# Kernel tuning notes

Hardware: AMD Instinct MI355X
Metric: run time of the kernel (lower is better)

The kernel has to match this reference:

```python
import jax, jax.numpy as jnp
import numpy as np

B, C, H, W = 256, 512, 14, 14
HW = H * W
TAU = 0.03          # args.tau
EPS = 0.65          # args.epsilon
EPS2 = 0.40         # args.epsilon - args.epsilon_margin
T_LOGIT = 0.07      # args.logit_temperature
MAX_ITERS = 32      # static unrolled bound for the data-dependent while-loop
PD_EPS = 1e-6       # torch.nn.PairwiseDistance default eps (added to the difference)


def setup_inputs() -> dict:
    key = jax.random.key(0)
    k1, k2 = jax.random.split(key)
    img = jax.random.normal(k1, (B, C, H, W), jnp.float32)
    img = img / (jnp.linalg.norm(img, axis=1, keepdims=True) + 1e-12)  # L2 over channels
    aud = jax.random.normal(k2, (B, C), jnp.float32)
    aud = aud / (jnp.linalg.norm(aud, axis=1, keepdims=True) + 1e-12)
    return {"img": img, "aud": aud}


def reference(img, aud):
    Bb, Cc, Hh, Ww = img.shape
    n_pix = Hh * Ww

    # PosLogits: [B,1,H,W]; Alllogits: [B,B,H,W]
    pos_logits = jnp.einsum('ncqa,nc->nqa', img, aud)[:, None]
    all_logits = jnp.einsum('ncqa,kc->nkqa', img, aud)

    # trimap negatives
    pos2 = jax.nn.sigmoid((pos_logits - EPS2) / TAU)
    neg = 1.0 - pos2                                        # [B,1,H,W]

    logit = img.reshape(Bb, Cc, -1) * pos_logits.reshape(Bb, 1, -1)   # [B,C,HW]
    positive0 = pos_logits.reshape(Bb, -1)                            # [B,HW]
    neg_val = (logit * neg.reshape(Bb, 1, -1)).mean(axis=2)           # [B,C]

    logit_t = logit.transpose(0, 2, 1)                                 # [B,HW,C]
    dist_to_zero = jnp.linalg.norm(logit_t - neg_val[:, None, :] + PD_EPS, axis=-1)  # [B,HW]

    def body(t, state):
        positive, already_pos, endpoint, obj = state
        idx = jnp.argmax(positive, axis=1)                             # [B] (detached in torch)
        sel = jnp.take_along_axis(logit, idx[:, None, None], axis=2)[:, :, 0]  # [B,C]
        obj = obj.at[t].set(sel * (~endpoint)[:, None].astype(sel.dtype))
        dist_to_logit = jnp.linalg.norm(logit_t - sel[:, None, :] + PD_EPS, axis=-1)  # [B,HW]
        pos = (dist_to_logit < dist_to_zero) & (~already_pos)
        already_pos = already_pos | pos
        positive = positive * (1.0 - pos.astype(positive.dtype))
        endpoint = endpoint | (pos.sum(axis=1) == 0) | (positive.max(axis=1) < 0.1)
        return (positive, already_pos, endpoint, obj)

    obj0 = jnp.zeros((MAX_ITERS, Bb, Cc), img.dtype)
    state0 = (positive0,
              jnp.zeros((Bb, n_pix), bool),
              jnp.zeros((Bb,), bool),
              obj0)
    _, _, _, object_arr = jax.lax.fori_loop(0, MAX_ITERS, body, state0)

    # lvs contrastive loss
    mask = 1.0 - 100.0 * jnp.eye(Bb, dtype=img.dtype)
    pos_m = jax.nn.sigmoid((pos_logits - EPS) / TAU)                   # [B,1,H,W]
    pos_all = jax.nn.sigmoid((all_logits - EPS) / TAU)                 # [B,B,H,W]
    sim1 = (pos_m * pos_logits).reshape(Bb, 1, -1).sum(-1) / pos_m.reshape(Bb, 1, -1).sum(-1)
    sim = (pos_all * all_logits).reshape(Bb, Bb, -1).sum(-1) / pos_all.reshape(Bb, Bb, -1).sum(-1) * mask
    sim2 = (neg * pos_logits).reshape(Bb, 1, -1).sum(-1) / neg.reshape(Bb, 1, -1).sum(-1)
    logits = jnp.concatenate((sim1, sim, sim2), axis=1) / T_LOGIT      # [B, B+2]
    loss = -jax.nn.log_softmax(logits, axis=1)[:, 0].mean()           # CE with target 0

    return loss, pos_logits[:, 0], object_arr
```

## Files before the change

kernel.cpp:

```cpp
#include <hip/hip_runtime.h>
#include <hip/hip_bf16.h>
#include <math.h>

#define NB 256
#define NC 512
#define NP 196
#define NIT 32
#define PROWS 208
#define PR 196
#define LSTR 72
#define SFSTR 211

typedef __attribute__((ext_vector_type(8))) short bf16x8;
typedef __attribute__((ext_vector_type(4))) float f32x4;

__device__ __forceinline__ float sigf(float z){ return 1.0f/(1.0f+expf(-z)); }

__device__ __forceinline__ unsigned short f2bf(float x){
  return __bfloat16_as_ushort(__float2bfloat16(x));
}
__device__ __forceinline__ float bf2f(unsigned short h){
  union{float f; unsigned u;} v; v.u = ((unsigned)h)<<16; return v.f;
}
__device__ __forceinline__ double dshfl_xor(double v, int m){
  int lo = __shfl_xor(__double2loint(v), m);
  int hi = __shfl_xor(__double2hiint(v), m);
  return __hiloint2double(hi, lo);
}


__global__ __launch_bounds__(512) void convert4_kernel(
    const float* __restrict__ img, const float* __restrict__ aud,
    unsigned short* __restrict__ hiT, unsigned short* __restrict__ loT,
    unsigned short* __restrict__ aud_bf,
    double* __restrict__ ppl, double* __restrict__ pcs)
{
  const int bid = blockIdx.x;
  const int b = bid & 255, part = bid >> 8;
  const int tid = threadIdx.x;
  const float* imgb = img + (size_t)b*NC*NP + (size_t)part*64*NP;
  __shared__ float sf[64*SFSTR];
  __shared__ float s_aud[64];
  if (part == 0) aud_bf[b*NC + tid] = f2bf(aud[b*NC + tid]);
  if (tid < 64) s_aud[tid] = aud[b*NC + part*64 + tid];

  for (int j=tid; j<64*49; j+=512){
    int p4 = j % 49, c = j / 49;
    float4 v = *(const float4*)&imgb[(size_t)c*NP + p4*4];
    sf[c*SFSTR + p4*4+0]=v.x; sf[c*SFSTR + p4*4+1]=v.y;
    sf[c*SFSTR + p4*4+2]=v.z; sf[c*SFSTR + p4*4+3]=v.w;
  }
  __syncthreads();

  unsigned short* hp = hiT + (size_t)(b*8+part)*PR*64;
  unsigned short* lp = loT + (size_t)(b*8+part)*PR*64;
  for (int j=tid; j<PROWS*8; j+=512){
    int p = j>>3, o = j&7;
    unsigned hw[4], lw[4];
    double dot=0.0, sm=0.0;
    #pragma unroll
    for (int k2=0;k2<4;++k2){
      int c = o*8 + 2*k2;
      float x0 = (p<NP) ? sf[c*SFSTR + p]     : 0.f;
      float x1 = (p<NP) ? sf[(c+1)*SFSTR + p] : 0.f;
      unsigned short h0=f2bf(x0), h1=f2bf(x1);
      unsigned short l0=f2bf(x0-bf2f(h0)), l1=f2bf(x1-bf2f(h1));
      hw[k2] = (unsigned)h0 | ((unsigned)h1<<16);
      lw[k2] = (unsigned)l0 | ((unsigned)l1<<16);
      dot += (double)x0*(double)s_aud[c] + (double)x1*(double)s_aud[c+1];
      sm  += (double)x0 + (double)x1;
    }
    if (p < NP){
      *(uint4*)&hp[p*64 + o*8] = *(uint4*)hw;
      *(uint4*)&lp[p*64 + o*8] = *(uint4*)lw;
    }
    dot += dshfl_xor(dot,1); dot += dshfl_xor(dot,2); dot += dshfl_xor(dot,4);
    sm  += dshfl_xor(sm,1);  sm  += dshfl_xor(sm,2);  sm  += dshfl_xor(sm,4);
    if (o==0 && p<NP){
      ppl[(size_t)(b*8+part)*NP + p] = dot;
      pcs[(size_t)(b*8+part)*NP + p] = sm;
    }
  }
}

__global__ __launch_bounds__(512) void gram2_kernel(
    const unsigned short* __restrict__ hiT, const unsigned short* __restrict__ loT,
    float* __restrict__ G)
{
  const int bid = blockIdx.x;
  const int slot = bid & 7, seq = bid >> 3;
  const int b = slot + 8*(seq>>1), h = seq & 1;
  const int cbase = 7*h, ncl = 7 - h;
  const int tid = threadIdx.x, lane = tid & 63, w = tid >> 6;
  const int nr = (w<5)?2:1;
  const unsigned short* hb = hiT + (size_t)b*8*PR*64;
  const unsigned short* lb = loT + (size_t)b*8*PR*64;
  float* Gb = G + (size_t)b*NP*NP;
  __shared__ short smh[PROWS*LSTR];
  __shared__ short sml[PROWS*LSTR];

  f32x4 acc[2][7];
  #pragma unroll
  for (int i=0;i<2;++i)
    #pragma unroll
    for (int j=0;j<7;++j) acc[i][j]=(f32x4){0,0,0,0};

  for (int sl=0; sl<8; ++sl){
    __syncthreads();
    for (int j=tid; j<PROWS*8; j+=512){
      int p = j>>3, o = j&7;
      size_t src = ((size_t)sl*PR + p)*64 + o*8;
      *(uint4*)&smh[p*LSTR + o*8] = *(const uint4*)(hb + src);
      *(uint4*)&sml[p*LSTR + o*8] = *(const uint4*)(lb + src);
    }
    __syncthreads();
    #pragma unroll
    for (int kk=0; kk<2; ++kk){
      bf16x8 Ah[2], Al[2];
      #pragma unroll
      for (int i=0;i<2;++i){
        if (i<nr){
          int r = (w + 8*i)*16 + (lane&15);
          Ah[i] = *(const bf16x8*)&smh[r*LSTR + kk*32 + (lane>>4)*8];
          Al[i] = *(const bf16x8*)&sml[r*LSTR + kk*32 + (lane>>4)*8];
        }
      }
      #pragma unroll
      for (int j=0;j<7;++j){
        if (j<ncl){
          int r = (cbase+j)*16 + (lane&15);
          bf16x8 Bh = *(const bf16x8*)&smh[r*LSTR + kk*32 + (lane>>4)*8];
          bf16x8 Bl = *(const bf16x8*)&sml[r*LSTR + kk*32 + (lane>>4)*8];
          #pragma unroll
          for (int i=0;i<2;++i){
            if (i<nr){
              acc[i][j] = __builtin_amdgcn_mfma_f32_16x16x32_bf16(Ah[i], Bh, acc[i][j], 0,0,0);
              acc[i][j] = __builtin_amdgcn_mfma_f32_16x16x32_bf16(Ah[i], Bl, acc[i][j], 0,0,0);
              acc[i][j] = __builtin_amdgcn_mfma_f32_16x16x32_bf16(Al[i], Bh, acc[i][j], 0,0,0);
            }
          }
        }
      }
    }
  }

  const int r0 = (lane>>4)*4, colL = lane & 15;
  #pragma unroll
  for (int i=0;i<2;++i){
    #pragma unroll
    for (int j=0;j<7;++j){
      if (i<nr && j<ncl){
        int row = (w+8*i)*16 + r0;
        int col = (cbase+j)*16 + colL;
        if (col < NP){
          #pragma unroll
          for (int jj=0;jj<4;++jj){
            if (row+jj < NP) Gb[(size_t)(row+jj)*NP + col] = acc[i][j][jj];
          }
        }
      }
    }
  }
}

__global__ __launch_bounds__(1024) void loop6_kernel(
    const double* __restrict__ ppl, const double* __restrict__ pcs,
    const float* __restrict__ G,
    const unsigned short* __restrict__ hiT, const unsigned short* __restrict__ loT,
    float* __restrict__ pl, float* __restrict__ out_pl,
    float* __restrict__ obj)
{
  const int b = blockIdx.x, tid = threadIdx.x, lane = tid & 63, w = tid >> 6;
  const float* Gb = G + (size_t)b*NP*NP;
  __shared__ float sG[NP*NP];
  __shared__ float s_pl[NP], s_wl[NP], s_csL[NP], s_gd[NP];
  __shared__ double gwd[NP];
  __shared__ double s_wred[16];
  __shared__ double s_bc;
  __shared__ int s_q[NIT]; __shared__ int s_z[NIT];

  #pragma unroll
  for (int k=0;k<10;++k){
    int j = k*1024 + tid;
    if (j < NP*NP/4) ((float4*)sG)[j] = ((const float4*)Gb)[j];
  }
  float negw_t = 0.f;
  if (tid < NP){
    double a=0.0, s=0.0;
    #pragma unroll
    for (int part=0; part<8; ++part){
      a += ppl[(size_t)(b*8+part)*NP + tid];
      s += pcs[(size_t)(b*8+part)*NP + tid];
    }
    float plv=(float)a;
    float csv=(float)s;
    pl[b*NP+tid]=plv; out_pl[b*NP+tid]=plv;
    s_pl[tid] = plv;
    s_csL[tid] = plv*csv;
    negw_t = 1.0f - sigf((plv-0.40f)/0.03f);
    s_wl[tid] = plv*negw_t;
    s_gd[tid] = Gb[(size_t)tid*NP + tid];
  }
  __syncthreads();

  {
    int p = tid >> 2, qg = tid & 3;
    double a = 0.0;
    if (p < NP){
      for (int q=qg*49; q<qg*49+49; ++q) a += (double)sG[q*NP + p] * (double)s_wl[q];
    }
    a += dshfl_xor(a,1); a += dshfl_xor(a,2);
    if (qg==0 && p<NP) gwd[p] = a;
  }
  __syncthreads();

  double r = (tid<NP) ? (double)s_wl[tid]*gwd[tid] : 0.0;
  #pragma unroll
  for (int m=1;m<64;m<<=1) r += dshfl_xor(r,m);
  if (lane==0) s_wred[w] = r;
  __syncthreads();
  if (tid==0){ double t=0.0; for (int i=0;i<16;++i) t += s_wred[i]; s_bc = t; }
  __syncthreads();
  const double S2 = s_bc;
  __syncthreads();

  r = (tid<NP) ? (double)negw_t*(double)s_csL[tid] : 0.0;
  #pragma unroll
  for (int m=1;m<64;m<<=1) r += dshfl_xor(r,m);
  if (lane==0) s_wred[w] = r;
  __syncthreads();
  if (tid==0){ double t=0.0; for (int i=0;i<16;++i) t += s_wred[i]; s_bc = t; }
  __syncthreads();
  const double Swl = s_bc;
  __syncthreads();

  if (tid < NP){
    const double e = (double)1e-6f;
    double pld = (double)s_pl[tid];
    double d0sq = pld*pld*(double)s_gd[tid]
                - (2.0/196.0)*pld*gwd[tid]
                + S2/(196.0*196.0)
                + 2.0*e*((double)s_csL[tid] - Swl/196.0)
                + 512.0*e*e;
    if (d0sq < 0.0) d0sq = 0.0;
    gwd[tid] = d0sq;
  }
  __syncthreads();

  if (w == 0){
    float plv[4], csL[4], gdd[4], posv[4];
    double d0sq[4];
    bool alr[4];
    #pragma unroll
    for (int s=0;s<4;++s){
      int p = lane + 64*s;
      bool valid = p < NP;
      plv[s]  = valid ? s_pl[p]  : 0.f;
      csL[s]  = valid ? s_csL[p] : 0.f;
      gdd[s]  = valid ? s_gd[p]  : 0.f;
      d0sq[s] = valid ? gwd[p]   : 0.0;
      posv[s] = valid ? plv[s]   : -INFINITY;
      alr[s] = false;
    }
    bool endp = false;

    for (int t=0;t<NIT;++t){
      float v = posv[0]; int ix = lane;
      #pragma unroll
      for (int s=1;s<4;++s){
        if (posv[s] > v){ v = posv[s]; ix = lane + 64*s; }
      }
      #pragma unroll
      for (int m=1;m<64;m<<=1){
        float vv = __shfl_xor(v, m);
        int   ii = __shfl_xor(ix, m);
        if (vv>v || (vv==v && ii<ix)){ v=vv; ix=ii; }
      }
      const int q = ix;
      const float plq  = s_pl[q];
      const float gqq  = s_gd[q];
      const float csLq = s_csL[q];
      if (lane==0){ s_q[t] = q; s_z[t] = endp ? 1 : 0; }

      int cnt = 0;
      #pragma unroll
      for (int s=0;s<4;++s){
        int p = lane + 64*s;
        if (p<NP && !alr[s]){
          float Gpq = sG[q*NP + p];
          double plp=(double)plv[s], dq=(double)plq;
          const double e=(double)1e-6f;
          double d2 = plp*plp*(double)gdd[s]
                    - 2.0*plp*dq*(double)Gpq
                    + dq*dq*(double)gqq
                    + 2.0*e*((double)csL[s]-(double)csLq)
                    + 512.0*e*e;
          if (d2<0.0) d2=0.0;
          if (d2 < d0sq[s]){ alr[s]=true; posv[s]=posv[s]*0.0f; cnt++; }
        }
      }
      float mx = fmaxf(fmaxf(posv[0],posv[1]),fmaxf(posv[2],posv[3]));
      #pragma unroll
      for (int m=1;m<64;m<<=1){
        cnt += __shfl_xor(cnt, m);
        mx = fmaxf(mx, __shfl_xor(mx, m));
      }
      if (cnt==0 || mx<0.1f) endp=true;
    }
  }
  __syncthreads();

  for (int j=tid; j<NIT*64; j+=1024){
    int t = j >> 6, l8 = j & 63;
    int part = l8 >> 3, off = l8 & 7;
    float o8[8];
    if (s_z[t]){
      #pragma unroll
      for (int e=0;e<8;++e) o8[e]=0.f;
    } else {
      int q = s_q[t];
      float plq = s_pl[q];
      size_t src = ((size_t)(b*8+part)*PR + q)*64 + off*8;
      uint4 hv = *(const uint4*)(hiT + src);
      uint4 lv = *(const uint4*)(loT + src);
      const unsigned* hw = (const unsigned*)&hv;
      const unsigned* lw = (const unsigned*)&lv;
      #pragma unroll
      for (int k2=0;k2<4;++k2){
        float x0 = bf2f((unsigned short)(hw[k2]&0xffff)) + bf2f((unsigned short)(lw[k2]&0xffff));
        float x1 = bf2f((unsigned short)(hw[k2]>>16))    + bf2f((unsigned short)(lw[k2]>>16));
        o8[2*k2]   = x0*plq;
        o8[2*k2+1] = x1*plq;
      }
    }
    float* op = obj + ((size_t)t*NB + b)*NC + l8*8;
    *(float4*)&op[0] = *(float4*)&o8[0];
    *(float4*)&op[4] = *(float4*)&o8[4];
  }
}

__global__ __launch_bounds__(512) void simgemm2_kernel(
    const unsigned short* __restrict__ hiT, const unsigned short* __restrict__ aud_bf,
    float* __restrict__ sumWA, float* __restrict__ sumW)
{
  const int bid = blockIdx.x;
  const int slot = bid & 7, seq = bid >> 3;
  const int b = slot + 8*(seq>>1), h = seq & 1;
  const int tid = threadIdx.x, lane = tid & 63, w = tid >> 6;
  const int wr = w >> 2, wc = w & 3;
  const int pbase = (wr==0)?0:7, npt = 7-wr;
  const unsigned short* hb = hiT + (size_t)b*8*PR*64;
  __shared__ short smh[PROWS*LSTR];
  __shared__ short sma[128*LSTR];
  __shared__ float sred[2][2][4][2][16];

  f32x4 acc[7][2];
  #pragma unroll
  for (int i=0;i<7;++i)
    #pragma unroll
    for (int n=0;n<2;++n) acc[i][n]=(f32x4){0,0,0,0};

  for (int sl=0; sl<8; ++sl){
    __syncthreads();
    for (int j=tid; j<PROWS*8; j+=512){
      int p = j>>3, o = j&7;
      *(uint4*)&smh[p*LSTR + o*8] = *(const uint4*)(hb + ((size_t)sl*PR + p)*64 + o*8);
    }
    for (int j=tid; j<128*8; j+=512){
      int n = j>>3, o = j&7;
      *(uint4*)&sma[n*LSTR + o*8] = *(const uint4*)(aud_bf + (size_t)(h*128+n)*NC + sl*64 + o*8);
    }
    __syncthreads();
    #pragma unroll
    for (int kk=0; kk<2; ++kk){
      bf16x8 Ah[7];
      #pragma unroll
      for (int i=0;i<7;++i){
        if (i<npt){
          int r = (pbase+i)*16 + (lane&15);
          Ah[i] = *(const bf16x8*)&smh[r*LSTR + kk*32 + (lane>>4)*8];
        }
      }
      #pragma unroll
      for (int n=0;n<2;++n){
        int r = (wc*2+n)*16 + (lane&15);
        bf16x8 Bn = *(const bf16x8*)&sma[r*LSTR + kk*32 + (lane>>4)*8];
        #pragma unroll
        for (int i=0;i<7;++i)
          if (i<npt)
            acc[i][n] = __builtin_amdgcn_mfma_f32_16x16x32_bf16(Ah[i], Bn, acc[i][n], 0,0,0);
      }
    }
  }

  float swa[2]={0,0}, sw[2]={0,0};
  #pragma unroll
  for (int n=0;n<2;++n){
    #pragma unroll
    for (int i=0;i<7;++i){
      if (i<npt){
        int rowbase = (pbase+i)*16 + (lane>>4)*4;
        #pragma unroll
        for (int jj=0;jj<4;++jj){
          if (rowbase+jj < NP){
            float v = acc[i][n][jj];
            float wgt = sigf((v-0.65f)/0.03f);
            swa[n] += wgt*v; sw[n] += wgt;
          }
        }
      }
    }
  }
  #pragma unroll
  for (int n=0;n<2;++n){
    swa[n] += __shfl_xor(swa[n],16); swa[n] += __shfl_xor(swa[n],32);
    sw[n]  += __shfl_xor(sw[n],16);  sw[n]  += __shfl_xor(sw[n],32);
  }
  if (lane < 16){
    #pragma unroll
    for (int n=0;n<2;++n){
      sred[0][wr][wc][n][lane] = swa[n];
      sred[1][wr][wc][n][lane] = sw[n];
    }
  }
  __syncthreads();
  if (tid < 128){
    int wc2 = tid>>5, n2 = (tid>>4)&1, col = tid&15;
    float a = sred[0][0][wc2][n2][col] + sred[0][1][wc2][n2][col];
    float s = sred[1][0][wc2][n2][col] + sred[1][1][wc2][n2][col];
    int kcol = h*128 + (wc2*2+n2)*16 + col;
    sumWA[(size_t)b*NB + kcol] = a;
    sumW [(size_t)b*NB + kcol] = s;
  }
}

__global__ __launch_bounds__(256) void finalize_b2(
    const float* __restrict__ pl,
    const float* __restrict__ sumWA, const float* __restrict__ sumW,
    float* __restrict__ lossb)
{
  const int b = blockIdx.x, k = threadIdx.x;
  __shared__ float s_red[256];
  __shared__ double s_redd[256];

  float plv = (k<NP)? pl[b*NP+k] : 0.f;
  float pmw = (k<NP)? sigf((plv-0.65f)/0.03f) : 0.f;
  float negw= (k<NP)? 1.0f - sigf((plv-0.40f)/0.03f) : 0.f;
  double rr[4];
  rr[0]=(k<NP)?(double)pmw*(double)plv:0.0;
  rr[1]=(k<NP)?(double)pmw:0.0;
  rr[2]=(k<NP)?(double)negw*(double)plv:0.0;
  rr[3]=(k<NP)?(double)negw:0.0;
  double res[4];
  for (int i=0;i<4;++i){
    __syncthreads();
    s_redd[k]=rr[i];
    __syncthreads();
    for (int s=128;s>0;s>>=1){ if (k<s) s_redd[k]+=s_redd[k+s]; __syncthreads(); }
    res[i]=s_redd[0];
  }
  const float sim1v = (float)(res[0]/res[1]);
  const float sim2v = (float)(res[2]/res[3]);
  __syncthreads();

  const float T = 0.07f;
  float s = sumWA[(size_t)b*NB+k]/sumW[(size_t)b*NB+k];
  if (k==b) s *= -99.0f;
  const float lk = s/T;
  const float l0 = sim1v/T, ll = sim2v/T;
  s_red[k]=lk; __syncthreads();
  for (int st=128;st>0;st>>=1){ if(k<st) s_red[k]=fmaxf(s_red[k],s_red[k+st]); __syncthreads(); }
  const float m = fmaxf(s_red[0], fmaxf(l0,ll));
  __syncthreads();
  double e = (double)expf(lk-m);
  if (k==0) e += (double)expf(l0-m)+(double)expf(ll-m);
  s_redd[k]=e; __syncthreads();
  for (int st=128;st>0;st>>=1){ if(k<st) s_redd[k]+=s_redd[k+st]; __syncthreads(); }
  if (k==0) lossb[b] = -(float)((double)(l0-m) - log(s_redd[0]));
}

__global__ __launch_bounds__(256) void finalize_sum(const float* __restrict__ lossb, float* __restrict__ out_loss)
{
  const int tid = threadIdx.x;
  __shared__ double sr[256];
  sr[tid]=(double)lossb[tid]; __syncthreads();
  for (int st=128;st>0;st>>=1){ if(tid<st) sr[tid]+=sr[tid+st]; __syncthreads(); }
  if (tid==0) out_loss[0]=(float)(sr[0]/256.0);
}

extern "C" void kernel_launch(void* const* d_in, const int* in_sizes, int n_in,
                              void* d_out, int out_size, void* d_ws, size_t ws_size,
                              hipStream_t stream)
{
  const float* img = (const float*)d_in[0];
  const float* aud = (const float*)d_in[1];
  float* out = (float*)d_out;
  float* ws  = (float*)d_ws;

  float* pl    = ws;
  unsigned short* aud_bf = (unsigned short*)(pl + NB*NP);
  unsigned short* hiT = aud_bf + NB*NC;
  unsigned short* loT = hiT + (size_t)NB*8*PR*64;
  float* G     = (float*)(loT + (size_t)NB*8*PR*64);
  double* ppl  = (double*)(G + (size_t)NB*NP*NP);
  double* pcs  = ppl + (size_t)NB*8*NP;
  float* lossb = (float*)(pcs + (size_t)NB*8*NP);

  float* sumWA = (float*)ppl;
  float* sumW  = sumWA + NB*NB;

  float* out_loss = out;
  float* out_pl   = out + 1;
  float* out_obj  = out + 1 + NB*NP;

  hipLaunchKernelGGL(convert4_kernel, dim3(NB*8),  dim3(512),  0, stream, img, aud, hiT, loT, aud_bf, ppl, pcs);
  hipLaunchKernelGGL(gram2_kernel,    dim3(NB*2),  dim3(512),  0, stream, hiT, loT, G);
  hipLaunchKernelGGL(loop6_kernel,    dim3(NB),    dim3(1024), 0, stream, ppl, pcs, G, hiT, loT, pl, out_pl, out_obj);
  hipLaunchKernelGGL(simgemm2_kernel, dim3(NB*2),  dim3(512),  0, stream, hiT, aud_bf, sumWA, sumW);
  hipLaunchKernelGGL(finalize_b2,     dim3(NB),    dim3(256),  0, stream, pl, sumWA, sumW, lossb);
  hipLaunchKernelGGL(finalize_sum,    dim3(1),     dim3(256),  0, stream, lossb, out_loss);
}
```

Before: 189.6 us.

## Fuse gram and similarity GEMMs into one kernel sharing staged hiT tiles

Merges the Gram-matrix GEMM and the audio-similarity GEMM into a single kernel that loads each hiT slice into LDS once and feeds both MFMA accumulations. This removes a separate kernel launch and a second full read of hiT from global memory. The sumWA/sumW buffers move to a dedicated workspace region since ppl is still live when they are written. The fused kernel holds more accumulators and LDS per block, which may reduce occupancy.

```diff
diff --git a/kernel.cpp b/kernel.cpp
--- a/kernel.cpp
+++ b/kernel.cpp
@@ -83,27 +83,37 @@
   }
 }
 
-__global__ __launch_bounds__(512) void gram2_kernel(
+__global__ __launch_bounds__(512) void gramsim3_kernel(
     const unsigned short* __restrict__ hiT, const unsigned short* __restrict__ loT,
-    float* __restrict__ G)
+    const unsigned short* __restrict__ aud_bf,
+    float* __restrict__ G, float* __restrict__ sumWA, float* __restrict__ sumW)
 {
   const int bid = blockIdx.x;
   const int slot = bid & 7, seq = bid >> 3;
   const int b = slot + 8*(seq>>1), h = seq & 1;
+  const int tid = threadIdx.x, lane = tid & 63, w = tid >> 6;
   const int cbase = 7*h, ncl = 7 - h;
-  const int tid = threadIdx.x, lane = tid & 63, w = tid >> 6;
   const int nr = (w<5)?2:1;
+  const int wr = w >> 2, wc = w & 3;
+  const int pbase = (wr==0)?0:7, npt = 7-wr;
   const unsigned short* hb = hiT + (size_t)b*8*PR*64;
   const unsigned short* lb = loT + (size_t)b*8*PR*64;
   float* Gb = G + (size_t)b*NP*NP;
   __shared__ short smh[PROWS*LSTR];
   __shared__ short sml[PROWS*LSTR];
-
-  f32x4 acc[2][7];
+  __shared__ short sma[128*LSTR];
+  __shared__ float sred[2][2][4][2][16];
+
+  f32x4 gacc[2][7];
   #pragma unroll
   for (int i=0;i<2;++i)
     #pragma unroll
-    for (int j=0;j<7;++j) acc[i][j]=(f32x4){0,0,0,0};
+    for (int j=0;j<7;++j) gacc[i][j]=(f32x4){0,0,0,0};
+  f32x4 sacc[7][2];
+  #pragma unroll
+  for (int i=0;i<7;++i)
+    #pragma unroll
+    for (int n=0;n<2;++n) sacc[i][n]=(f32x4){0,0,0,0};
 
   for (int sl=0; sl<8; ++sl){
     __syncthreads();
@@ -113,53 +123,120 @@
       *(uint4*)&smh[p*LSTR + o*8] = *(const uint4*)(hb + src);
       *(uint4*)&sml[p*LSTR + o*8] = *(const uint4*)(lb + src);
     }
+    for (int j=tid; j<128*8; j+=512){
+      int n = j>>3, o = j&7;
+      *(uint4*)&sma[n*LSTR + o*8] = *(const uint4*)(aud_bf + (size_t)(h*128+n)*NC + sl*64 + o*8);
+    }
     __syncthreads();
     #pragma unroll
     for (int kk=0; kk<2; ++kk){
-      bf16x8 Ah[2], Al[2];
-      #pragma unroll
-      for (int i=0;i<2;++i){
-        if (i<nr){
-          int r = (w + 8*i)*16 + (lane&15);
-          Ah[i] = *(const bf16x8*)&smh[r*LSTR + kk*32 + (lane>>4)*8];
-          Al[i] = *(const bf16x8*)&sml[r*LSTR + kk*32 + (lane>>4)*8];
-        }
-      }
-      #pragma unroll
-      for (int j=0;j<7;++j){
-        if (j<ncl){
-          int r = (cbase+j)*16 + (lane&15);
-          bf16x8 Bh = *(const bf16x8*)&smh[r*LSTR + kk*32 + (lane>>4)*8];
-          bf16x8 Bl = *(const bf16x8*)&sml[r*LSTR + kk*32 + (lane>>4)*8];
-          #pragma unroll
-          for (int i=0;i<2;++i){
-            if (i<nr){
-              acc[i][j] = __builtin_amdgcn_mfma_f32_16x16x32_bf16(Ah[i], Bh, acc[i][j], 0,0,0);
-              acc[i][j] = __builtin_amdgcn_mfma_f32_16x16x32_bf16(Ah[i], Bl, acc[i][j], 0,0,0);
-              acc[i][j] = __builtin_amdgcn_mfma_f32_16x16x32_bf16(Al[i], Bh, acc[i][j], 0,0,0);
+      {
+        bf16x8 Ah[2], Al[2];
+        #pragma unroll
+        for (int i=0;i<2;++i){
+          if (i<nr){
+            int r = (w + 8*i)*16 + (lane&15);
+            Ah[i] = *(const bf16x8*)&smh[r*LSTR + kk*32 + (lane>>4)*8];
+            Al[i] = *(const bf16x8*)&sml[r*LSTR + kk*32 + (lane>>4)*8];
+          }
+        }
+        #pragma unroll
+        for (int j=0;j<7;++j){
+          if (j<ncl){
+            int r = (cbase+j)*16 + (lane&15);
+            bf16x8 Bh = *(const bf16x8*)&smh[r*LSTR + kk*32 + (lane>>4)*8];
+            bf16x8 Bl = *(const bf16x8*)&sml[r*LSTR + kk*32 + (lane>>4)*8];
+            #pragma unroll
+            for (int i=0;i<2;++i){
+              if (i<nr){
+                gacc[i][j] = __builtin_amdgcn_mfma_f32_16x16x32_bf16(Ah[i], Bh, gacc[i][j], 0,0,0);
+                gacc[i][j] = __builtin_amdgcn_mfma_f32_16x16x32_bf16(Ah[i], Bl, gacc[i][j], 0,0,0);
+                gacc[i][j] = __builtin_amdgcn_mfma_f32_16x16x32_bf16(Al[i], Bh, gacc[i][j], 0,0,0);
+              }
             }
           }
         }
       }
-    }
-  }
-
-  const int r0 = (lane>>4)*4, colL = lane & 15;
-  #pragma unroll
-  for (int i=0;i<2;++i){
-    #pragma unroll
-    for (int j=0;j<7;++j){
-      if (i<nr && j<ncl){
-        int row = (w+8*i)*16 + r0;
-        int col = (cbase+j)*16 + colL;
-        if (col < NP){
+      {
+        bf16x8 Ah[7];
+        #pragma unroll
+        for (int i=0;i<7;++i){
+          if (i<npt){
+            int r = (pbase+i)*16 + (lane&15);
+            Ah[i] = *(const bf16x8*)&smh[r*LSTR + kk*32 + (lane>>4)*8];
+          }
+        }
+        #pragma unroll
+        for (int n=0;n<2;++n){
+          int r = (wc*2+n)*16 + (lane&15);
+          bf16x8 Bn = *(const bf16x8*)&sma[r*LSTR + kk*32 + (lane>>4)*8];
           #pragma unroll
-          for (int jj=0;jj<4;++jj){
-            if (row+jj < NP) Gb[(size_t)(row+jj)*NP + col] = acc[i][j][jj];
+          for (int i=0;i<7;++i)
+            if (i<npt)
+              sacc[i][n] = __builtin_amdgcn_mfma_f32_16x16x32_bf16(Ah[i], Bn, sacc[i][n], 0,0,0);
+        }
+      }
+    }
+  }
+
+  {
+    const int r0 = (lane>>4)*4, colL = lane & 15;
+    #pragma unroll
+    for (int i=0;i<2;++i){
+      #pragma unroll
+      for (int j=0;j<7;++j){
+        if (i<nr && j<ncl){
+          int row = (w+8*i)*16 + r0;
+          int col = (cbase+j)*16 + colL;
+          if (col < NP){
+            #pragma unroll
+            for (int jj=0;jj<4;++jj){
+              if (row+jj < NP) Gb[(size_t)(row+jj)*NP + col] = gacc[i][j][jj];
+            }
           }
         }
       }
     }
+  }
+
+  float swa[2]={0,0}, sw[2]={0,0};
+  #pragma unroll
+  for (int n=0;n<2;++n){
+    #pragma unroll
+    for (int i=0;i<7;++i){
+      if (i<npt){
+        int rowbase = (pbase+i)*16 + (lane>>4)*4;
+        #pragma unroll
+        for (int jj=0;jj<4;++jj){
+          if (rowbase+jj < NP){
+            float v = sacc[i][n][jj];
+            float wgt = sigf((v-0.65f)/0.03f);
+            swa[n] += wgt*v; sw[n] += wgt;
+          }
+        }
+      }
+    }
+  }
+  #pragma unroll
+  for (int n=0;n<2;++n){
+    swa[n] += __shfl_xor(swa[n],16); swa[n] += __shfl_xor(swa[n],32);
+    sw[n]  += __shfl_xor(sw[n],16);  sw[n]  += __shfl_xor(sw[n],32);
+  }
+  if (lane < 16){
+    #pragma unroll
+    for (int n=0;n<2;++n){
+      sred[0][wr][wc][n][lane] = swa[n];
+      sred[1][wr][wc][n][lane] = sw[n];
+    }
+  }
+  __syncthreads();
+  if (tid < 128){
+    int wc2 = tid>>5, n2 = (tid>>4)&1, col = tid&15;
+    float a = sred[0][0][wc2][n2][col] + sred[0][1][wc2][n2][col];
+    float s = sred[1][0][wc2][n2][col] + sred[1][1][wc2][n2][col];
+    int kcol = h*128 + (wc2*2+n2)*16 + col;
+    sumWA[(size_t)b*NB + kcol] = a;
+    sumW [(size_t)b*NB + kcol] = s;
   }
 }
 
@@ -339,101 +416,6 @@
   }
 }
 
-__global__ __launch_bounds__(512) void simgemm2_kernel(
-    const unsigned short* __restrict__ hiT, const unsigned short* __restrict__ aud_bf,
-    float* __restrict__ sumWA, float* __restrict__ sumW)
-{
-  const int bid = blockIdx.x;
-  const int slot = bid & 7, seq = bid >> 3;
-  const int b = slot + 8*(seq>>1), h = seq & 1;
-  const int tid = threadIdx.x, lane = tid & 63, w = tid >> 6;
-  const int wr = w >> 2, wc = w & 3;
-  const int pbase = (wr==0)?0:7, npt = 7-wr;
-  const unsigned short* hb = hiT + (size_t)b*8*PR*64;
-  __shared__ short smh[PROWS*LSTR];
-  __shared__ short sma[128*LSTR];
-  __shared__ float sred[2][2][4][2][16];
-
-  f32x4 acc[7][2];
-  #pragma unroll
-  for (int i=0;i<7;++i)
-    #pragma unroll
-    for (int n=0;n<2;++n) acc[i][n]=(f32x4){0,0,0,0};
-
-  for (int sl=0; sl<8; ++sl){
-    __syncthreads();
-    for (int j=tid; j<PROWS*8; j+=512){
-      int p = j>>3, o = j&7;
-      *(uint4*)&smh[p*LSTR + o*8] = *(const uint4*)(hb + ((size_t)sl*PR + p)*64 + o*8);
-    }
-    for (int j=tid; j<128*8; j+=512){
-      int n = j>>3, o = j&7;
-      *(uint4*)&sma[n*LSTR + o*8] = *(const uint4*)(aud_bf + (size_t)(h*128+n)*NC + sl*64 + o*8);
-    }
-    __syncthreads();
-    #pragma unroll
-    for (int kk=0; kk<2; ++kk){
-      bf16x8 Ah[7];
-      #pragma unroll
-      for (int i=0;i<7;++i){
-        if (i<npt){
-          int r = (pbase+i)*16 + (lane&15);
-          Ah[i] = *(const bf16x8*)&smh[r*LSTR + kk*32 + (lane>>4)*8];
-        }
-      }
-      #pragma unroll
-      for (int n=0;n<2;++n){
-        int r = (wc*2+n)*16 + (lane&15);
-        bf16x8 Bn = *(const bf16x8*)&sma[r*LSTR + kk*32 + (lane>>4)*8];
-        #pragma unroll
-        for (int i=0;i<7;++i)
-          if (i<npt)
-            acc[i][n] = __builtin_amdgcn_mfma_f32_16x16x32_bf16(Ah[i], Bn, acc[i][n], 0,0,0);
-      }
-    }
-  }
-
-  float swa[2]={0,0}, sw[2]={0,0};
-  #pragma unroll
-  for (int n=0;n<2;++n){
-    #pragma unroll
-    for (int i=0;i<7;++i){
-      if (i<npt){
-        int rowbase = (pbase+i)*16 + (lane>>4)*4;
-        #pragma unroll
-        for (int jj=0;jj<4;++jj){
-          if (rowbase+jj < NP){
-            float v = acc[i][n][jj];
-            float wgt = sigf((v-0.65f)/0.03f);
-            swa[n] += wgt*v; sw[n] += wgt;
-          }
-        }
-      }
-    }
-  }
-  #pragma unroll
-  for (int n=0;n<2;++n){
-    swa[n] += __shfl_xor(swa[n],16); swa[n] += __shfl_xor(swa[n],32);
-    sw[n]  += __shfl_xor(sw[n],16);  sw[n]  += __shfl_xor(sw[n],32);
-  }
-  if (lane < 16){
-    #pragma unroll
-    for (int n=0;n<2;++n){
-      sred[0][wr][wc][n][lane] = swa[n];
-      sred[1][wr][wc][n][lane] = sw[n];
-    }
-  }
-  __syncthreads();
-  if (tid < 128){
-    int wc2 = tid>>5, n2 = (tid>>4)&1, col = tid&15;
-    float a = sred[0][0][wc2][n2][col] + sred[0][1][wc2][n2][col];
-    float s = sred[1][0][wc2][n2][col] + sred[1][1][wc2][n2][col];
-    int kcol = h*128 + (wc2*2+n2)*16 + col;
-    sumWA[(size_t)b*NB + kcol] = a;
-    sumW [(size_t)b*NB + kcol] = s;
-  }
-}
-
 __global__ __launch_bounds__(256) void finalize_b2(
     const float* __restrict__ pl,
     const float* __restrict__ sumWA, const float* __restrict__ sumW,
@@ -506,7 +488,7 @@
   double* pcs  = ppl + (size_t)NB*8*NP;
   float* lossb = (float*)(pcs + (size_t)NB*8*NP);
 
-  float* sumWA = (float*)ppl;
+  float* sumWA = lossb + NB;
   float* sumW  = sumWA + NB*NB;
 
   float* out_loss = out;
@@ -514,9 +496,8 @@
   float* out_obj  = out + 1 + NB*NP;
 
   hipLaunchKernelGGL(convert4_kernel, dim3(NB*8),  dim3(512),  0, stream, img, aud, hiT, loT, aud_bf, ppl, pcs);
-  hipLaunchKernelGGL(gram2_kernel,    dim3(NB*2),  dim3(512),  0, stream, hiT, loT, G);
+  hipLaunchKernelGGL(gramsim3_kernel, dim3(NB*2),  dim3(512),  0, stream, hiT, loT, aud_bf, G, sumWA, sumW);
   hipLaunchKernelGGL(loop6_kernel,    dim3(NB),    dim3(1024), 0, stream, ppl, pcs, G, hiT, loT, pl, out_pl, out_obj);
-  hipLaunchKernelGGL(simgemm2_kernel, dim3(NB*2),  dim3(512),  0, stream, hiT, aud_bf, sumWA, sumW);
   hipLaunchKernelGGL(finalize_b2,     dim3(NB),    dim3(256),  0, stream, pl, sumWA, sumW, lossb);
   hipLaunchKernelGGL(finalize_sum,    dim3(1),     dim3(256),  0, stream, lossb, out_loss);
 }
```

Result: slower. 210.0 us (+10.7%).
